# Kernel optimization log

Measured on AMD Instinct MI355X. Metric: run time of the kernel, lower is better.

The kernel has to match this reference:

```python
import jax, jax.numpy as jnp
import numpy as np

NEG_SLOPE = 0.2  # PyG GATConv default LeakyReLU slope


def gat_conv(x, src, dst, W, a_src, a_dst, b):
    """Single-head GATConv (PyG defaults: heads=1, add_self_loops already done).
    x: [N, F_in]; src/dst: [E] int (self loops included); W: [F_in, F_out];
    a_src, a_dst: [F_out]; b: [F_out].
    """
    N = x.shape[0]
    h = x @ W                           # [N, F_out]
    alpha_src = h @ a_src               # [N]
    alpha_dst = h @ a_dst               # [N]
    e = alpha_src[src] + alpha_dst[dst]  # [E]
    e = jnp.where(e > 0, e, NEG_SLOPE * e)  # LeakyReLU
    # numerically stable segment softmax over edges grouped by dst
    m = jax.ops.segment_max(e, dst, num_segments=N)      # [N]
    ex = jnp.exp(e - m[dst])                             # [E]
    denom = jax.ops.segment_sum(ex, dst, num_segments=N)  # [N]
    alpha = ex / denom[dst]                              # [E]
    out = jax.ops.segment_sum(alpha[:, None] * h[src], dst, num_segments=N)
    return out + b


def add_self_loops(edge_index, N):
    loop = jnp.arange(N, dtype=edge_index.dtype)
    src = jnp.concatenate([edge_index[0], loop])
    dst = jnp.concatenate([edge_index[1], loop])
    return src, dst


def setup_inputs() -> dict:
    key = jax.random.key(0)
    N, E = 100000, 1600000
    dims = [128, 128, 128, 128]  # in -> hidden0 -> hidden1 -> out
    ks = jax.random.split(key, 16)
    inp = {
        "x": jax.random.normal(ks[0], (N, dims[0]), dtype=jnp.float32),
        "edge_index": jax.random.randint(ks[1], (2, E), 0, N, dtype=jnp.int32),
    }
    ki = 2
    for l in range(3):
        fi, fo = dims[l], dims[l + 1]
        inp[f"W{l}"] = jax.random.normal(ks[ki], (fi, fo), dtype=jnp.float32) * (1.0 / np.sqrt(fi)); ki += 1
        inp[f"a_src{l}"] = jax.random.normal(ks[ki], (fo,), dtype=jnp.float32) * 0.1; ki += 1
        inp[f"a_dst{l}"] = jax.random.normal(ks[ki], (fo,), dtype=jnp.float32) * 0.1; ki += 1
        inp[f"b{l}"] = jnp.zeros((fo,), dtype=jnp.float32); ki += 1
    return inp


def reference(x, edge_index,
              W0, a_src0, a_dst0, b0,
              W1, a_src1, a_dst1, b1,
              W2, a_src2, a_dst2, b2):
    N = x.shape[0]
    src, dst = add_self_loops(edge_index, N)
    h = gat_conv(x, src, dst, W0, a_src0, a_dst0, b0)
    h = jax.nn.elu(h)
    h = gat_conv(h, src, dst, W1, a_src1, a_dst1, b1)
    h = jax.nn.elu(h)
    out = gat_conv(h, src, dst, W2, a_src2, a_dst2, b2)
    return out
```

## Files before the change

### kernel.cpp

```cpp
#include <hip/hip_runtime.h>
#include <hip/hip_bf16.h>
#include <hip/hip_fp16.h>
#include <math.h>

#define NEG_SLOPE 0.2f

typedef unsigned int uint;
typedef __bf16 bf16x8 __attribute__((ext_vector_type(8)));
typedef __bf16 bf16x4 __attribute__((ext_vector_type(4)));
typedef __bf16 bf16x2 __attribute__((ext_vector_type(2)));
typedef _Float16 f16x2 __attribute__((ext_vector_type(2)));
typedef float floatx4 __attribute__((ext_vector_type(4)));

#define CPAD 5

__device__ inline float2 h2_to_f2(uint v) {
    f16x2 p = __builtin_bit_cast(f16x2, v);
    return make_float2((float)p[0], (float)p[1]);
}


__global__ void count_deg_rank(const int* __restrict__ dst, int* __restrict__ deg,
                               int* __restrict__ rank, int E) {
    int t = blockIdx.x * blockDim.x + threadIdx.x;
    int stride = gridDim.x * blockDim.x;
    int E4 = E >> 2;
    for (int i4 = t; i4 < E4; i4 += stride) {
        int4 d4 = ((const int4*)dst)[i4];
        int4 r4;
        r4.x = atomicAdd(&deg[d4.x << CPAD], 1);
        r4.y = atomicAdd(&deg[d4.y << CPAD], 1);
        r4.z = atomicAdd(&deg[d4.z << CPAD], 1);
        r4.w = atomicAdd(&deg[d4.w << CPAD], 1);
        ((int4*)rank)[i4] = r4;
    }
    for (int i = (E4 << 2) + t; i < E; i += stride)
        rank[i] = atomicAdd(&deg[dst[i] << CPAD], 1);
}

__global__ void scan_block_k(const int* __restrict__ deg, int* __restrict__ off,
                             int* __restrict__ bsum, int N) {
    __shared__ int sdata[256];
    int t = threadIdx.x;
    int base = blockIdx.x * 1024 + t * 4;
    int v0 = (base + 0 < N) ? deg[(base + 0) << CPAD] : 0;
    int v1 = (base + 1 < N) ? deg[(base + 1) << CPAD] : 0;
    int v2 = (base + 2 < N) ? deg[(base + 2) << CPAD] : 0;
    int v3 = (base + 3 < N) ? deg[(base + 3) << CPAD] : 0;
    int s = v0 + v1 + v2 + v3;
    sdata[t] = s;
    __syncthreads();
    for (int d = 1; d < 256; d <<= 1) {
        int x = (t >= d) ? sdata[t - d] : 0;
        __syncthreads();
        sdata[t] += x;
        __syncthreads();
    }
    int run = sdata[t] - s;
    if (t == 255) bsum[blockIdx.x] = sdata[255];
    if (base + 0 < N) off[base + 0] = run; run += v0;
    if (base + 1 < N) off[base + 1] = run; run += v1;
    if (base + 2 < N) off[base + 2] = run; run += v2;
    if (base + 3 < N) off[base + 3] = run;
}

__global__ void scan_bsum_k(int* bsum, int G) {
    __shared__ int sdata[1024];
    int t = threadIdx.x;
    int v = (t < G) ? bsum[t] : 0;
    sdata[t] = v;
    __syncthreads();
    for (int d = 1; d < 1024; d <<= 1) {
        int x = (t >= d) ? sdata[t - d] : 0;
        __syncthreads();
        sdata[t] += x;
        __syncthreads();
    }
    if (t < G) bsum[t] = sdata[t] - v;
}

__global__ void add_bsum_k(int* __restrict__ off, const int* __restrict__ bsum,
                           int N, int Etot) {
    int i = blockIdx.x * blockDim.x + threadIdx.x;
    if (i < N) off[i] += bsum[i >> 10];
    else if (i == N) off[N] = Etot;
}

__global__ void fill_scatter(const int* __restrict__ src, const int* __restrict__ dst,
                             const int* __restrict__ rank, const int* __restrict__ off,
                             int* __restrict__ csr_src, int E) {
    int t = blockIdx.x * blockDim.x + threadIdx.x;
    int stride = gridDim.x * blockDim.x;
    int E4 = E >> 2;
    for (int i4 = t; i4 < E4; i4 += stride) {
        int4 d4 = ((const int4*)dst)[i4];
        int4 s4 = ((const int4*)src)[i4];
        int4 r4 = ((const int4*)rank)[i4];
        csr_src[off[d4.x] + r4.x] = s4.x;
        csr_src[off[d4.y] + r4.y] = s4.y;
        csr_src[off[d4.z] + r4.z] = s4.z;
        csr_src[off[d4.w] + r4.w] = s4.w;
    }
    for (int i = (E4 << 2) + t; i < E; i += stride)
        csr_src[off[dst[i]] + rank[i]] = src[i];
}


__global__ void split_x_k(const float* __restrict__ in, __bf16* __restrict__ hi,
                          __bf16* __restrict__ lo, int n4) {
    int i = blockIdx.x * blockDim.x + threadIdx.x;
    if (i >= n4) return;
    float4 v = ((const float4*)in)[i];
    bf16x4 h = { (__bf16)v.x, (__bf16)v.y, (__bf16)v.z, (__bf16)v.w };
    bf16x4 l = { (__bf16)(v.x - (float)h[0]), (__bf16)(v.y - (float)h[1]),
                 (__bf16)(v.z - (float)h[2]), (__bf16)(v.w - (float)h[3]) };
    ((bf16x4*)hi)[i] = h;
    ((bf16x4*)lo)[i] = l;
}

__global__ void split_w_k(const float* __restrict__ W0, const float* __restrict__ W1,
                          const float* __restrict__ W2, __bf16* __restrict__ Wfh,
                          __bf16* __restrict__ Wfl) {
    const float* W = (blockIdx.y == 0) ? W0 : (blockIdx.y == 1) ? W1 : W2;
    size_t base = (size_t)blockIdx.y * 16384;
    int i = blockIdx.x * 256 + threadIdx.x;
    int k = i >> 7, ncol = i & 127;
    int ct = ncol >> 4, n16 = ncol & 15;
    int kt = k >> 5, q = (k & 31) >> 3, j = k & 7;
    size_t flat = (size_t)(((ct * 4 + kt) * 64) + q * 16 + n16) * 8 + j;
    float v = W[i];
    __bf16 h = (__bf16)v;
    __bf16 l = (__bf16)(v - (float)h);
    Wfh[base + flat] = h;
    Wfl[base + flat] = l;
}


__global__ __launch_bounds__(256, 2) void gemm_split(
    const __bf16* __restrict__ Ah, const __bf16* __restrict__ Al,
    const __bf16* __restrict__ Wh, const __bf16* __restrict__ Wl,
    const float* __restrict__ avs, const float* __restrict__ avd,
    _Float16* __restrict__ Hh, float* __restrict__ asrc, float* __restrict__ adst,
    int M) {
    __shared__ __align__(16) char lds_raw[65536];
    int tid = threadIdx.x;
    int wv = tid >> 6, lane = tid & 63;
    int n = lane & 15, q = lane >> 4;

    #pragma unroll
    for (int it = 0; it < 16; ++it) {
        int boff = it * 4096 + tid * 16;
        const char* s = (it < 8) ? ((const char*)Wh + boff)
                                 : ((const char*)Wl + (boff - 32768));
        *(float4*)(lds_raw + boff) = *(const float4*)s;
    }

    int arow_g = blockIdx.x * 64 + wv * 16 + n;
    int arow_c = (arow_g < M) ? arow_g : (M - 1);
    const bf16x8* ah = (const bf16x8*)(Ah + (size_t)arow_c * 128);
    const bf16x8* al = (const bf16x8*)(Al + (size_t)arow_c * 128);
    bf16x8 a_h[4], a_l[4];
    #pragma unroll
    for (int kt = 0; kt < 4; ++kt) {
        a_h[kt] = ah[kt * 4 + q];
        a_l[kt] = al[kt * 4 + q];
    }
    __syncthreads();

    floatx4 acc[8];
    #pragma unroll
    for (int ct = 0; ct < 8; ++ct) {
        floatx4 c = {0.f, 0.f, 0.f, 0.f};
        #pragma unroll
        for (int kt = 0; kt < 4; ++kt) {
            int fo = ((ct * 4 + kt) * 64 + lane) * 16;
            bf16x8 bh = *(const bf16x8*)(lds_raw + fo);
            bf16x8 bl = *(const bf16x8*)(lds_raw + 32768 + fo);
            c = __builtin_amdgcn_mfma_f32_16x16x32_bf16(a_h[kt], bh, c, 0, 0, 0);
            c = __builtin_amdgcn_mfma_f32_16x16x32_bf16(a_h[kt], bl, c, 0, 0, 0);
            c = __builtin_amdgcn_mfma_f32_16x16x32_bf16(a_l[kt], bh, c, 0, 0, 0);
        }
        acc[ct] = c;
    }

    float ps[4] = {0.f, 0.f, 0.f, 0.f}, pd[4] = {0.f, 0.f, 0.f, 0.f};
    #pragma unroll
    for (int ct = 0; ct < 8; ++ct) {
        float sv = avs[ct * 16 + n], dv = avd[ct * 16 + n];
        #pragma unroll
        for (int r = 0; r < 4; ++r) {
            ps[r] += acc[ct][r] * sv;
            pd[r] += acc[ct][r] * dv;
        }
    }
    #pragma unroll
    for (int m = 1; m < 16; m <<= 1) {
        #pragma unroll
        for (int r = 0; r < 4; ++r) {
            ps[r] += __shfl_xor(ps[r], m, 64);
            pd[r] += __shfl_xor(pd[r], m, 64);
        }
    }
    if (n == 0) {
        #pragma unroll
        for (int r = 0; r < 4; ++r) {
            int grow = blockIdx.x * 64 + wv * 16 + q * 4 + r;
            if (grow < M) { asrc[grow] = ps[r]; adst[grow] = pd[r]; }
        }
    }

    __syncthreads();
    _Float16 (*hl)[132] = (_Float16(*)[132])lds_raw;
    #pragma unroll
    for (int ct = 0; ct < 8; ++ct)
        #pragma unroll
        for (int r = 0; r < 4; ++r)
            hl[wv * 16 + q * 4 + r][ct * 16 + n] = (_Float16)acc[ct][r];
    __syncthreads();

    int r0 = blockIdx.x * 64;
    for (int i = tid; i < 64 * 64; i += 256) {
        int rr = i >> 6, cu = i & 63;
        int gr = r0 + rr;
        if (gr < M)
            ((uint*)Hh)[(size_t)gr * 64 + cu] = *(const uint*)&hl[rr][cu * 2];
    }
}


__global__ __launch_bounds__(256) void edge_w_k(
    const float* __restrict__ asrc, const float* __restrict__ adst,
    const int* __restrict__ off, const int* __restrict__ csr_src,
    float* __restrict__ ew, float* __restrict__ wself, int N) {
    int gid = blockIdx.x * blockDim.x + threadIdx.x;
    int wave = gid >> 6, lane = gid & 63;
    int node = wave * 4 + (lane >> 4);
    int l16 = lane & 15;
    if (node >= N) return;
    float ad = adst[node];
    int beg = off[node], end = off[node + 1];
    if (l16 == 0) {
        float e = asrc[node] + ad;
        e = (e > 0.f) ? e : NEG_SLOPE * e;
        wself[node] = __expf(e);
    }
    for (int p = beg + l16; p < end; p += 16) {
        float e = asrc[csr_src[p]] + ad;
        e = (e > 0.f) ? e : NEG_SLOPE * e;
        ew[p] = __expf(e);
    }
}


template <int FINAL>
__global__ __launch_bounds__(256) void aggregate_k(
    const _Float16* __restrict__ h, const float* __restrict__ ew,
    const float* __restrict__ wself, const int* __restrict__ off,
    const int* __restrict__ csr_src, const float* __restrict__ bias,
    float* __restrict__ out_f, __bf16* __restrict__ a_hi, __bf16* __restrict__ a_lo,
    int N, int E) {
    int gid = blockIdx.x * blockDim.x + threadIdx.x;
    int wid = gid >> 6, lane = gid & 63;
    if (wid >= N) return;
    const uint* hrows = (const uint*)h;
    float acc0, acc1, denom;

    {
        float w = wself[wid];
        float2 f = h2_to_f2(hrows[(size_t)wid * 64 + lane]);
        denom = w; acc0 = w * f.x; acc1 = w * f.y;
    }

    int beg = __builtin_amdgcn_readfirstlane(off[wid]);
    int end = __builtin_amdgcn_readfirstlane(off[wid + 1]);
    int Em1 = E - 1;
    for (int j = beg; j < end; j += 4) {
        int i1 = j + 1, i2 = j + 2, i3 = j + 3;
        int c1 = (i1 < E) ? i1 : Em1;
        int c2 = (i2 < E) ? i2 : Em1;
        int c3 = (i3 < E) ? i3 : Em1;
        int s0 = __builtin_amdgcn_readfirstlane(csr_src[j]);
        int s1 = __builtin_amdgcn_readfirstlane(csr_src[c1]);
        int s2 = __builtin_amdgcn_readfirstlane(csr_src[c2]);
        int s3 = __builtin_amdgcn_readfirstlane(csr_src[c3]);
        const uint* r0 = hrows + (size_t)s0 * 64;
        const uint* r1 = hrows + (size_t)s1 * 64;
        const uint* r2 = hrows + (size_t)s2 * 64;
        const uint* r3 = hrows + (size_t)s3 * 64;
        uint v0 = r0[lane];
        uint v1 = r1[lane];
        uint v2 = r2[lane];
        uint v3 = r3[lane];
        float w0 = ew[j];
        float w1 = ew[c1];
        float w2 = ew[c2];
        float w3 = ew[c3];
        w1 = (i1 < end) ? w1 : 0.f;
        w2 = (i2 < end) ? w2 : 0.f;
        w3 = (i3 < end) ? w3 : 0.f;
        denom += (w0 + w1) + (w2 + w3);
        float2 f0 = h2_to_f2(v0), f1 = h2_to_f2(v1);
        float2 f2 = h2_to_f2(v2), f3 = h2_to_f2(v3);
        acc0 += w0 * f0.x + w1 * f1.x + w2 * f2.x + w3 * f3.x;
        acc1 += w0 * f0.y + w1 * f1.y + w2 * f2.y + w3 * f3.y;
    }

    float inv = 1.0f / denom;
    float2 b2 = ((const float2*)bias)[lane];
    float o0 = acc0 * inv + b2.x;
    float o1 = acc1 * inv + b2.y;
    if (FINAL) {
        ((float2*)out_f)[(size_t)wid * 64 + lane] = make_float2(o0, o1);
    } else {
        o0 = (o0 > 0.f) ? o0 : (__expf(o0) - 1.0f);
        o1 = (o1 > 0.f) ? o1 : (__expf(o1) - 1.0f);
        __bf16 h0 = (__bf16)o0, h1 = (__bf16)o1;
        bf16x2 ph = { h0, h1 };
        bf16x2 pl = { (__bf16)(o0 - (float)h0), (__bf16)(o1 - (float)h1) };
        ((bf16x2*)a_hi)[(size_t)wid * 64 + lane] = ph;
        ((bf16x2*)a_lo)[(size_t)wid * 64 + lane] = pl;
    }
}


extern "C" void kernel_launch(void* const* d_in, const int* in_sizes, int n_in,
                              void* d_out, int out_size, void* d_ws, size_t ws_size,
                              hipStream_t stream) {
    const float* x = (const float*)d_in[0];
    const int* ei = (const int*)d_in[1];
    int N = in_sizes[0] / 128;
    int E = in_sizes[1] / 2;
    const int* src = ei;
    const int* dst = ei + E;

    const float* Wl_[3] = { (const float*)d_in[2], (const float*)d_in[6], (const float*)d_in[10] };
    const float* asl[3] = { (const float*)d_in[3], (const float*)d_in[7], (const float*)d_in[11] };
    const float* adl[3] = { (const float*)d_in[4], (const float*)d_in[8], (const float*)d_in[12] };
    const float* bl[3]  = { (const float*)d_in[5], (const float*)d_in[9], (const float*)d_in[13] };

    size_t nfeat = (size_t)N * 128;
    char* p = (char*)d_ws;
    _Float16* Hh = (_Float16*)p; p += nfeat * 2;
    __bf16* Wfh = (__bf16*)p; p += 3 * 16384 * 2;
    __bf16* Wfl = (__bf16*)p; p += 3 * 16384 * 2;
    float* asrc = (float*)p;  p += (size_t)N * 4;
    float* adst = (float*)p;  p += (size_t)N * 4;
    int* off    = (int*)p;    p += (size_t)(N + 1) * 4;
    int* bsum   = (int*)p;    p += 4096 * 4;
    float* ew    = (float*)p; p += (size_t)E * 4;
    float* wself = (float*)p; p += (size_t)N * 4;
    int* csr    = (int*)p;

    int* cpad = (int*)Hh;
    int* rank = (int*)((char*)Hh + ((size_t)N << CPAD) * sizeof(int) / 1);

    __bf16* A_hi = (__bf16*)d_out;
    __bf16* A_lo = A_hi + nfeat;

    int G = (N + 1023) / 1024;

    hipMemsetAsync(cpad, 0, ((size_t)N << CPAD) * sizeof(int), stream);
    count_deg_rank<<<2048, 256, 0, stream>>>(dst, cpad, rank, E);
    scan_block_k<<<G, 256, 0, stream>>>(cpad, off, bsum, N);
    scan_bsum_k<<<1, 1024, 0, stream>>>(bsum, G);
    add_bsum_k<<<(N + 256) / 256, 256, 0, stream>>>(off, bsum, N, E);
    fill_scatter<<<2048, 256, 0, stream>>>(src, dst, rank, off, csr, E);

    split_w_k<<<dim3(64, 3), 256, 0, stream>>>(Wl_[0], Wl_[1], Wl_[2], Wfh, Wfl);
    int n4 = (int)(nfeat / 4);
    split_x_k<<<(n4 + 255) / 256, 256, 0, stream>>>(x, A_hi, A_lo, n4);

    int gemm_blocks = (N + 63) / 64;
    int wave_blocks = (N + 3) / 4;
    int ew_blocks = (N + 15) / 16;

    for (int l = 0; l < 3; ++l) {
        gemm_split<<<gemm_blocks, 256, 0, stream>>>(
            A_hi, A_lo, Wfh + (size_t)l * 16384, Wfl + (size_t)l * 16384,
            asl[l], adl[l], Hh, asrc, adst, N);
        edge_w_k<<<ew_blocks, 256, 0, stream>>>(asrc, adst, off, csr, ew, wself, N);
        if (l < 2) {
            aggregate_k<0><<<wave_blocks, 256, 0, stream>>>(
                Hh, ew, wself, off, csr, bl[l], nullptr, A_hi, A_lo, N, E);
        } else {
            aggregate_k<1><<<wave_blocks, 256, 0, stream>>>(
                Hh, ew, wself, off, csr, bl[l], (float*)d_out, nullptr, nullptr, N, E);
        }
    }
}
```

Baseline: 546.0 us.

## Interleave edge weights with CSR sources and prefetch next edge batch in aggregation

Stores the edge weight and source index together as an int2 pair array instead of two separate arrays. The aggregation loop now loads the next four (weight, source) pairs one iteration ahead, so index fetches overlap with feature row gathers. This cuts the separate index and weight loads and shortens the dependent load chain. In exchange, edge_w_k must read and rewrite 8-byte pairs, and the loop holds extra prefetch registers.

Result: no change. 553.5 us (+1.4%).

```diff
diff --git a/kernel.cpp b/kernel.cpp
--- a/kernel.cpp
+++ b/kernel.cpp
@@ -88,7 +88,7 @@
 
 __global__ void fill_scatter(const int* __restrict__ src, const int* __restrict__ dst,
                              const int* __restrict__ rank, const int* __restrict__ off,
-                             int* __restrict__ csr_src, int E) {
+                             int* __restrict__ pair_raw, int E) {
     int t = blockIdx.x * blockDim.x + threadIdx.x;
     int stride = gridDim.x * blockDim.x;
     int E4 = E >> 2;
@@ -96,13 +96,13 @@
         int4 d4 = ((const int4*)dst)[i4];
         int4 s4 = ((const int4*)src)[i4];
         int4 r4 = ((const int4*)rank)[i4];
-        csr_src[off[d4.x] + r4.x] = s4.x;
-        csr_src[off[d4.y] + r4.y] = s4.y;
-        csr_src[off[d4.z] + r4.z] = s4.z;
-        csr_src[off[d4.w] + r4.w] = s4.w;
+        pair_raw[((off[d4.x] + r4.x) << 1) + 1] = s4.x;
+        pair_raw[((off[d4.y] + r4.y) << 1) + 1] = s4.y;
+        pair_raw[((off[d4.z] + r4.z) << 1) + 1] = s4.z;
+        pair_raw[((off[d4.w] + r4.w) << 1) + 1] = s4.w;
     }
     for (int i = (E4 << 2) + t; i < E; i += stride)
-        csr_src[off[dst[i]] + rank[i]] = src[i];
+        pair_raw[((off[dst[i]] + rank[i]) << 1) + 1] = src[i];
 }
 
 
@@ -230,8 +230,8 @@
 
 __global__ __launch_bounds__(256) void edge_w_k(
     const float* __restrict__ asrc, const float* __restrict__ adst,
-    const int* __restrict__ off, const int* __restrict__ csr_src,
-    float* __restrict__ ew, float* __restrict__ wself, int N) {
+    const int* __restrict__ off, int2* __restrict__ ewp,
+    float* __restrict__ wself, int N) {
     int gid = blockIdx.x * blockDim.x + threadIdx.x;
     int wave = gid >> 6, lane = gid & 63;
     int node = wave * 4 + (lane >> 4);
@@ -245,18 +245,19 @@
         wself[node] = __expf(e);
     }
     for (int p = beg + l16; p < end; p += 16) {
-        float e = asrc[csr_src[p]] + ad;
+        int s = ewp[p].y;
+        float e = asrc[s] + ad;
         e = (e > 0.f) ? e : NEG_SLOPE * e;
-        ew[p] = __expf(e);
+        ewp[p] = make_int2(__float_as_int(__expf(e)), s);
     }
 }
 
 
 template <int FINAL>
 __global__ __launch_bounds__(256) void aggregate_k(
-    const _Float16* __restrict__ h, const float* __restrict__ ew,
+    const _Float16* __restrict__ h, const int2* __restrict__ ewp,
     const float* __restrict__ wself, const int* __restrict__ off,
-    const int* __restrict__ csr_src, const float* __restrict__ bias,
+    const float* __restrict__ bias,
     float* __restrict__ out_f, __bf16* __restrict__ a_hi, __bf16* __restrict__ a_lo,
     int N, int E) {
     int gid = blockIdx.x * blockDim.x + threadIdx.x;
@@ -274,35 +275,40 @@
     int beg = __builtin_amdgcn_readfirstlane(off[wid]);
     int end = __builtin_amdgcn_readfirstlane(off[wid + 1]);
     int Em1 = E - 1;
+
+    int2 q0 = ewp[(beg + 0 <= Em1) ? beg + 0 : Em1];
+    int2 q1 = ewp[(beg + 1 <= Em1) ? beg + 1 : Em1];
+    int2 q2 = ewp[(beg + 2 <= Em1) ? beg + 2 : Em1];
+    int2 q3 = ewp[(beg + 3 <= Em1) ? beg + 3 : Em1];
+
     for (int j = beg; j < end; j += 4) {
-        int i1 = j + 1, i2 = j + 2, i3 = j + 3;
-        int c1 = (i1 < E) ? i1 : Em1;
-        int c2 = (i2 < E) ? i2 : Em1;
-        int c3 = (i3 < E) ? i3 : Em1;
-        int s0 = __builtin_amdgcn_readfirstlane(csr_src[j]);
-        int s1 = __builtin_amdgcn_readfirstlane(csr_src[c1]);
-        int s2 = __builtin_amdgcn_readfirstlane(csr_src[c2]);
-        int s3 = __builtin_amdgcn_readfirstlane(csr_src[c3]);
-        const uint* r0 = hrows + (size_t)s0 * 64;
-        const uint* r1 = hrows + (size_t)s1 * 64;
-        const uint* r2 = hrows + (size_t)s2 * 64;
-        const uint* r3 = hrows + (size_t)s3 * 64;
-        uint v0 = r0[lane];
-        uint v1 = r1[lane];
-        uint v2 = r2[lane];
-        uint v3 = r3[lane];
-        float w0 = ew[j];
-        float w1 = ew[c1];
-        float w2 = ew[c2];
-        float w3 = ew[c3];
-        w1 = (i1 < end) ? w1 : 0.f;
-        w2 = (i2 < end) ? w2 : 0.f;
-        w3 = (i3 < end) ? w3 : 0.f;
+        int jn = j + 4;
+        int2 n0 = ewp[(jn + 0 <= Em1) ? jn + 0 : Em1];
+        int2 n1 = ewp[(jn + 1 <= Em1) ? jn + 1 : Em1];
+        int2 n2 = ewp[(jn + 2 <= Em1) ? jn + 2 : Em1];
+        int2 n3 = ewp[(jn + 3 <= Em1) ? jn + 3 : Em1];
+
+        int s0 = __builtin_amdgcn_readfirstlane(q0.y);
+        int s1 = __builtin_amdgcn_readfirstlane(q1.y);
+        int s2 = __builtin_amdgcn_readfirstlane(q2.y);
+        int s3 = __builtin_amdgcn_readfirstlane(q3.y);
+        uint v0 = hrows[(size_t)s0 * 64 + lane];
+        uint v1 = hrows[(size_t)s1 * 64 + lane];
+        uint v2 = hrows[(size_t)s2 * 64 + lane];
+        uint v3 = hrows[(size_t)s3 * 64 + lane];
+
+        float w0 = __int_as_float(q0.x);
+        float w1 = (j + 1 < end) ? __int_as_float(q1.x) : 0.f;
+        float w2 = (j + 2 < end) ? __int_as_float(q2.x) : 0.f;
+        float w3 = (j + 3 < end) ? __int_as_float(q3.x) : 0.f;
+
         denom += (w0 + w1) + (w2 + w3);
         float2 f0 = h2_to_f2(v0), f1 = h2_to_f2(v1);
         float2 f2 = h2_to_f2(v2), f3 = h2_to_f2(v3);
         acc0 += w0 * f0.x + w1 * f1.x + w2 * f2.x + w3 * f3.x;
         acc1 += w0 * f0.y + w1 * f1.y + w2 * f2.y + w3 * f3.y;
+
+        q0 = n0; q1 = n1; q2 = n2; q3 = n3;
     }
 
     float inv = 1.0f / denom;
@@ -347,12 +353,11 @@
     float* adst = (float*)p;  p += (size_t)N * 4;
     int* off    = (int*)p;    p += (size_t)(N + 1) * 4;
     int* bsum   = (int*)p;    p += 4096 * 4;
-    float* ew    = (float*)p; p += (size_t)E * 4;
     float* wself = (float*)p; p += (size_t)N * 4;
-    int* csr    = (int*)p;
+    int2* ewp   = (int2*)p;   p += (size_t)E * 8;
 
     int* cpad = (int*)Hh;
-    int* rank = (int*)((char*)Hh + ((size_t)N << CPAD) * sizeof(int) / 1);
+    int* rank = (int*)((char*)Hh + ((size_t)N << CPAD) * sizeof(int));
 
     __bf16* A_hi = (__bf16*)d_out;
     __bf16* A_lo = A_hi + nfeat;
@@ -364,7 +369,7 @@
     scan_block_k<<<G, 256, 0, stream>>>(cpad, off, bsum, N);
     scan_bsum_k<<<1, 1024, 0, stream>>>(bsum, G);
     add_bsum_k<<<(N + 256) / 256, 256, 0, stream>>>(off, bsum, N, E);
-    fill_scatter<<<2048, 256, 0, stream>>>(src, dst, rank, off, csr, E);
+    fill_scatter<<<2048, 256, 0, stream>>>(src, dst, rank, off, (int*)ewp, E);
 
     split_w_k<<<dim3(64, 3), 256, 0, stream>>>(Wl_[0], Wl_[1], Wl_[2], Wfh, Wfl);
     int n4 = (int)(nfeat / 4);
@@ -378,13 +383,13 @@
         gemm_split<<<gemm_blocks, 256, 0, stream>>>(
             A_hi, A_lo, Wfh + (size_t)l * 16384, Wfl + (size_t)l * 16384,
             asl[l], adl[l], Hh, asrc, adst, N);
-        edge_w_k<<<ew_blocks, 256, 0, stream>>>(asrc, adst, off, csr, ew, wself, N);
+        edge_w_k<<<ew_blocks, 256, 0, stream>>>(asrc, adst, off, ewp, wself, N);
         if (l < 2) {
             aggregate_k<0><<<wave_blocks, 256, 0, stream>>>(
-                Hh, ew, wself, off, csr, bl[l], nullptr, A_hi, A_lo, N, E);
+                Hh, ewp, wself, off, bl[l], nullptr, A_hi, A_lo, N, E);
         } else {
             aggregate_k<1><<<wave_blocks, 256, 0, stream>>>(
-                Hh, ew, wself, off, csr, bl[l], (float*)d_out, nullptr, nullptr, N, E);
-        }
-    }
-}
+                Hh, ewp, wself, off, bl[l], (float*)d_out, nullptr, nullptr, N, E);
+        }
+    }
+}
```

## Fuse edge-weight computation into aggregation via per-wave LDS staging

Applied to the files above, without the earlier changes.

Removes the separate edge_w_k kernel and its ew/wself buffers. The aggregation kernel now computes the exponentiated attention logits itself: each wave cooperatively loads a chunk of up to 128 neighbor indices, computes the weights, stages them with the source ids in LDS, then gathers feature rows 8 at a time instead of 4. This cuts one launch per layer and the write and re-read of the edge-weight array, and raises memory-level parallelism in the gather. In exchange it adds LDS traffic and per-chunk overhead, and relies on wave-local LDS ordering with only an s_waitcnt and no barrier.

Result: faster. 503.8 us (-7.7%).

```diff
diff --git a/kernel.cpp b/kernel.cpp
--- a/kernel.cpp
+++ b/kernel.cpp
@@ -228,81 +228,95 @@
 }
 
 
-__global__ __launch_bounds__(256) void edge_w_k(
-    const float* __restrict__ asrc, const float* __restrict__ adst,
-    const int* __restrict__ off, const int* __restrict__ csr_src,
-    float* __restrict__ ew, float* __restrict__ wself, int N) {
-    int gid = blockIdx.x * blockDim.x + threadIdx.x;
-    int wave = gid >> 6, lane = gid & 63;
-    int node = wave * 4 + (lane >> 4);
-    int l16 = lane & 15;
-    if (node >= N) return;
-    float ad = adst[node];
-    int beg = off[node], end = off[node + 1];
-    if (l16 == 0) {
-        float e = asrc[node] + ad;
-        e = (e > 0.f) ? e : NEG_SLOPE * e;
-        wself[node] = __expf(e);
-    }
-    for (int p = beg + l16; p < end; p += 16) {
-        float e = asrc[csr_src[p]] + ad;
-        e = (e > 0.f) ? e : NEG_SLOPE * e;
-        ew[p] = __expf(e);
-    }
-}
-
+#define EW_CAP 128
 
 template <int FINAL>
 __global__ __launch_bounds__(256) void aggregate_k(
-    const _Float16* __restrict__ h, const float* __restrict__ ew,
-    const float* __restrict__ wself, const int* __restrict__ off,
-    const int* __restrict__ csr_src, const float* __restrict__ bias,
+    const _Float16* __restrict__ h, const float* __restrict__ asrc,
+    const float* __restrict__ adst, const int* __restrict__ off,
+    const int* __restrict__ csr, const float* __restrict__ bias,
     float* __restrict__ out_f, __bf16* __restrict__ a_hi, __bf16* __restrict__ a_lo,
     int N, int E) {
+    __shared__ int2 srec[4][EW_CAP];
     int gid = blockIdx.x * blockDim.x + threadIdx.x;
     int wid = gid >> 6, lane = gid & 63;
+    int wv = (threadIdx.x >> 6);
     if (wid >= N) return;
     const uint* hrows = (const uint*)h;
+    float ad = adst[wid];
     float acc0, acc1, denom;
 
     {
-        float w = wself[wid];
+        float e = asrc[wid] + ad;
+        e = (e > 0.f) ? e : NEG_SLOPE * e;
+        float w = __expf(e);
         float2 f = h2_to_f2(hrows[(size_t)wid * 64 + lane]);
         denom = w; acc0 = w * f.x; acc1 = w * f.y;
     }
 
     int beg = __builtin_amdgcn_readfirstlane(off[wid]);
     int end = __builtin_amdgcn_readfirstlane(off[wid + 1]);
-    int Em1 = E - 1;
-    for (int j = beg; j < end; j += 4) {
-        int i1 = j + 1, i2 = j + 2, i3 = j + 3;
-        int c1 = (i1 < E) ? i1 : Em1;
-        int c2 = (i2 < E) ? i2 : Em1;
-        int c3 = (i3 < E) ? i3 : Em1;
-        int s0 = __builtin_amdgcn_readfirstlane(csr_src[j]);
-        int s1 = __builtin_amdgcn_readfirstlane(csr_src[c1]);
-        int s2 = __builtin_amdgcn_readfirstlane(csr_src[c2]);
-        int s3 = __builtin_amdgcn_readfirstlane(csr_src[c3]);
-        const uint* r0 = hrows + (size_t)s0 * 64;
-        const uint* r1 = hrows + (size_t)s1 * 64;
-        const uint* r2 = hrows + (size_t)s2 * 64;
-        const uint* r3 = hrows + (size_t)s3 * 64;
-        uint v0 = r0[lane];
-        uint v1 = r1[lane];
-        uint v2 = r2[lane];
-        uint v3 = r3[lane];
-        float w0 = ew[j];
-        float w1 = ew[c1];
-        float w2 = ew[c2];
-        float w3 = ew[c3];
-        w1 = (i1 < end) ? w1 : 0.f;
-        w2 = (i2 < end) ? w2 : 0.f;
-        w3 = (i3 < end) ? w3 : 0.f;
-        denom += (w0 + w1) + (w2 + w3);
-        float2 f0 = h2_to_f2(v0), f1 = h2_to_f2(v1);
-        float2 f2 = h2_to_f2(v2), f3 = h2_to_f2(v3);
-        acc0 += w0 * f0.x + w1 * f1.x + w2 * f2.x + w3 * f3.x;
-        acc1 += w0 * f0.y + w1 * f1.y + w2 * f2.y + w3 * f3.y;
+
+    for (int sc = beg; sc < end; sc += EW_CAP) {
+        int cnt = end - sc; cnt = (cnt < EW_CAP) ? cnt : EW_CAP;
+
+        for (int e0 = lane; e0 < cnt; e0 += 64) {
+            int s = csr[sc + e0];
+            float e = asrc[s] + ad;
+            e = (e > 0.f) ? e : NEG_SLOPE * e;
+            srec[wv][e0] = make_int2(__float_as_int(__expf(e)), s);
+        }
+        asm volatile("s_waitcnt lgkmcnt(0)" ::: "memory");
+
+        int cm1 = cnt - 1;
+        for (int j = 0; j < cnt; j += 8) {
+            int2 r0 = srec[wv][j];
+            int2 r1 = srec[wv][(j + 1 <= cm1) ? j + 1 : cm1];
+            int2 r2 = srec[wv][(j + 2 <= cm1) ? j + 2 : cm1];
+            int2 r3 = srec[wv][(j + 3 <= cm1) ? j + 3 : cm1];
+            int2 r4 = srec[wv][(j + 4 <= cm1) ? j + 4 : cm1];
+            int2 r5 = srec[wv][(j + 5 <= cm1) ? j + 5 : cm1];
+            int2 r6 = srec[wv][(j + 6 <= cm1) ? j + 6 : cm1];
+            int2 r7 = srec[wv][(j + 7 <= cm1) ? j + 7 : cm1];
+            int s0 = __builtin_amdgcn_readfirstlane(r0.y);
+            int s1 = __builtin_amdgcn_readfirstlane(r1.y);
+            int s2 = __builtin_amdgcn_readfirstlane(r2.y);
+            int s3 = __builtin_amdgcn_readfirstlane(r3.y);
+            int s4 = __builtin_amdgcn_readfirstlane(r4.y);
+            int s5 = __builtin_amdgcn_readfirstlane(r5.y);
+            int s6 = __builtin_amdgcn_readfirstlane(r6.y);
+            int s7 = __builtin_amdgcn_readfirstlane(r7.y);
+            uint v0 = hrows[(size_t)s0 * 64 + lane];
+            uint v1 = hrows[(size_t)s1 * 64 + lane];
+            uint v2 = hrows[(size_t)s2 * 64 + lane];
+            uint v3 = hrows[(size_t)s3 * 64 + lane];
+            uint v4 = hrows[(size_t)s4 * 64 + lane];
+            uint v5 = hrows[(size_t)s5 * 64 + lane];
+            uint v6 = hrows[(size_t)s6 * 64 + lane];
+            uint v7 = hrows[(size_t)s7 * 64 + lane];
+
+            float w0 = __int_as_float(r0.x);
+            float w1 = (j + 1 < cnt) ? __int_as_float(r1.x) : 0.f;
+            float w2 = (j + 2 < cnt) ? __int_as_float(r2.x) : 0.f;
+            float w3 = (j + 3 < cnt) ? __int_as_float(r3.x) : 0.f;
+            float w4 = (j + 4 < cnt) ? __int_as_float(r4.x) : 0.f;
+            float w5 = (j + 5 < cnt) ? __int_as_float(r5.x) : 0.f;
+            float w6 = (j + 6 < cnt) ? __int_as_float(r6.x) : 0.f;
+            float w7 = (j + 7 < cnt) ? __int_as_float(r7.x) : 0.f;
+
+            denom += (w0 + w1) + (w2 + w3);
+            float2 f0 = h2_to_f2(v0), f1 = h2_to_f2(v1);
+            float2 f2 = h2_to_f2(v2), f3 = h2_to_f2(v3);
+            acc0 += w0 * f0.x + w1 * f1.x + w2 * f2.x + w3 * f3.x;
+            acc1 += w0 * f0.y + w1 * f1.y + w2 * f2.y + w3 * f3.y;
+
+            denom += (w4 + w5) + (w6 + w7);
+            float2 f4 = h2_to_f2(v4), f5 = h2_to_f2(v5);
+            float2 f6 = h2_to_f2(v6), f7 = h2_to_f2(v7);
+            acc0 += w4 * f4.x + w5 * f5.x + w6 * f6.x + w7 * f7.x;
+            acc1 += w4 * f4.y + w5 * f5.y + w6 * f6.y + w7 * f7.y;
+        }
+        asm volatile("s_waitcnt lgkmcnt(0)" ::: "memory");
     }
 
     float inv = 1.0f / denom;
@@ -347,12 +361,10 @@
     float* adst = (float*)p;  p += (size_t)N * 4;
     int* off    = (int*)p;    p += (size_t)(N + 1) * 4;
     int* bsum   = (int*)p;    p += 4096 * 4;
-    float* ew    = (float*)p; p += (size_t)E * 4;
-    float* wself = (float*)p; p += (size_t)N * 4;
-    int* csr    = (int*)p;
+    int* csr    = (int*)p;    p += (size_t)E * 4;
 
     int* cpad = (int*)Hh;
-    int* rank = (int*)((char*)Hh + ((size_t)N << CPAD) * sizeof(int) / 1);
+    int* rank = (int*)((char*)Hh + ((size_t)N << CPAD) * sizeof(int));
 
     __bf16* A_hi = (__bf16*)d_out;
     __bf16* A_lo = A_hi + nfeat;
@@ -372,19 +384,17 @@
 
     int gemm_blocks = (N + 63) / 64;
     int wave_blocks = (N + 3) / 4;
-    int ew_blocks = (N + 15) / 16;
 
     for (int l = 0; l < 3; ++l) {
         gemm_split<<<gemm_blocks, 256, 0, stream>>>(
             A_hi, A_lo, Wfh + (size_t)l * 16384, Wfl + (size_t)l * 16384,
             asl[l], adl[l], Hh, asrc, adst, N);
-        edge_w_k<<<ew_blocks, 256, 0, stream>>>(asrc, adst, off, csr, ew, wself, N);
         if (l < 2) {
             aggregate_k<0><<<wave_blocks, 256, 0, stream>>>(
-                Hh, ew, wself, off, csr, bl[l], nullptr, A_hi, A_lo, N, E);
+                Hh, asrc, adst, off, csr, bl[l], nullptr, A_hi, A_lo, N, E);
         } else {
             aggregate_k<1><<<wave_blocks, 256, 0, stream>>>(
-                Hh, ew, wself, off, csr, bl[l], (float*)d_out, nullptr, nullptr, N, E);
-        }
-    }
-}
+                Hh, asrc, adst, off, csr, bl[l], (float*)d_out, nullptr, nullptr, N, E);
+        }
+    }
+}
```
